# Performance work log

Hardware: AMD Instinct MI355X
Metric: run time of the kernel (lower is better)

## Reference

```python
import jax, jax.numpy as jnp
import numpy as np

CODE_DIM = 512
N_CODES = 8192
COMMITMENT_WEIGHT = 1.0


def setup_inputs() -> dict:
    key = jax.random.key(0)
    kx, kc = jax.random.split(key)
    x = jax.random.normal(kx, (8, 2048, CODE_DIM), dtype=jnp.float32)
    codebook = jax.random.normal(kc, (N_CODES, CODE_DIM), dtype=jnp.float32)  # N(0,1) init as in torch
    return {"x": x, "codebook": codebook}


def _cdist(x, codebook):
    x2 = jnp.sum(x * x, axis=-1, keepdims=True)          # [B, T, 1]
    c2 = jnp.sum(codebook * codebook, axis=-1)           # [K]
    xc = jnp.einsum('btd,kd->btk', x, codebook)          # [B, T, K]
    sq = jnp.maximum(x2 + c2[None, None, :] - 2.0 * xc, 0.0)
    return jnp.sqrt(sq)


def reference(x, codebook):
    dist = _cdist(x, codebook)                           # [B, T, K]
    indices = jnp.argmin(dist, axis=-1)                  # [B, T]
    codes = codebook[indices]                            # [B, T, D]
    code_loss = jnp.mean((codes - jax.lax.stop_gradient(x)) ** 2)
    embedding_loss = jnp.mean((x - jax.lax.stop_gradient(codes)) ** 2) * COMMITMENT_WEIGHT
    loss = code_loss + embedding_loss
    quantized = x + jax.lax.stop_gradient(codes - x)     # straight-through estimator
    return (quantized, indices, loss)
```

## Files before the change

kernel.cpp:

```cpp
#include <hip/hip_runtime.h>
#include <hip/hip_bf16.h>

typedef signed char s8;
typedef unsigned int u32;
typedef unsigned long long u64;
typedef __attribute__((ext_vector_type(4))) int v4i;

#define M_TOK 16384
#define DDIM 512
#define NCODES 8192
#define NTILE 64
#define BKB 64
#define KCH 8

#define QS   25.4f
#define QINV (1.0f / (QS * QS))

#define OFF_A8   0u
#define OFF_B8   8388608u
#define OFF_PART 12582912u
#define OFF_C2   20971520u
#define OFF_ACC  21004288u

__global__ void zero_kernel(float* __restrict__ acc) {
    if (threadIdx.x == 0 && blockIdx.x == 0) *acc = 0.f;
}

__global__ void quant_cb_c2_kernel(const float* __restrict__ cb, s8* __restrict__ B8,
                                   float* __restrict__ c2) {
    int row  = blockIdx.x * 4 + (threadIdx.x >> 6);
    int l    = threadIdx.x & 63;
    const float* p = cb + (size_t)row * DDIM + l * 8;
    float4 a = *(const float4*)p;
    float4 b = *(const float4*)(p + 4);
    float v[8] = {a.x, a.y, a.z, a.w, b.x, b.y, b.z, b.w};
    union { s8 c[8]; uint2 q; } H;
    float s = 0.f;
    #pragma unroll
    for (int j = 0; j < 8; ++j) {
        int q = (int)rintf(fminf(fmaxf(v[j] * QS, -127.f), 127.f));
        H.c[j] = (s8)q;
        s += v[j] * v[j];
    }
    *(uint2*)(B8 + (size_t)row * DDIM + l * 8) = H.q;
    #pragma unroll
    for (int off = 32; off; off >>= 1) s += __shfl_down(s, off);
    if (l == 0) c2[row] = s;
}

__global__ void quant_x_kernel(const float* __restrict__ src, s8* __restrict__ dst, int n16) {
    int i = blockIdx.x * blockDim.x + threadIdx.x;
    if (i >= n16) return;
    const float4* s4 = (const float4*)src + (size_t)i * 4;
    union { s8 c[16]; uint4 q; } H;
    #pragma unroll
    for (int k = 0; k < 4; ++k) {
        float4 a = s4[k];
        float v[4] = {a.x, a.y, a.z, a.w};
        #pragma unroll
        for (int j = 0; j < 4; ++j) {
            int q = (int)rintf(fminf(fmaxf(v[j] * QS, -127.f), 127.f));
            H.c[k * 4 + j] = (s8)q;
        }
    }
    *(uint4*)(dst + (size_t)i * 16) = H.q;
}

__launch_bounds__(256, 4)
__global__ void gemm_top1_kernel(const s8* __restrict__ A8, const s8* __restrict__ B8,
                                 const float* __restrict__ c2, u64* __restrict__ part) {
    __shared__ __align__(16) s8 Asb[2][128 * BKB];
    __shared__ __align__(16) s8 Bsb[2][128 * BKB];
    __shared__ u64 mergebuf[128][2];

    const int tid = threadIdx.x;
    const int wid = tid >> 6;
    const int l   = tid & 63;
    const int wr  = wid >> 1, wc = wid & 1;
    const int mtile = blockIdx.x >> 6;
    const int ntile = blockIdx.x & 63;
    const int row0 = mtile * 128;
    const int col0 = ntile * 128;

    const int lg = l >> 4;
    const int lc = l & 15;

    const int srowoff = l >> 2;
    const int sslot   = (l & 3) ^ ((l >> 3) & 3);

    auto STAGE = [&](int buf, int kc) {
        const int k0 = kc * BKB;
        #pragma unroll
        for (int i = 0; i < 2; ++i) {
            int rbase = i * 64 + wid * 16;
            int row = rbase + srowoff;
            const s8* ga = A8 + (size_t)(row0 + row) * DDIM + k0 + sslot * 16;
            __builtin_amdgcn_global_load_lds(
                (const __attribute__((address_space(1))) void*)ga,
                (__attribute__((address_space(3))) void*)&Asb[buf][rbase * BKB], 16, 0, 0);
            const s8* gb = B8 + (size_t)(col0 + row) * DDIM + k0 + sslot * 16;
            __builtin_amdgcn_global_load_lds(
                (const __attribute__((address_space(1))) void*)gb,
                (__attribute__((address_space(3))) void*)&Bsb[buf][rbase * BKB], 16, 0, 0);
        }
    };

    v4i acc[4][4];
    #pragma unroll
    for (int m = 0; m < 4; ++m)
        #pragma unroll
        for (int n = 0; n < 4; ++n) acc[m][n] = (v4i){0, 0, 0, 0};

    STAGE(0, 0);
    int cur = 0;
    const int slotbyte = (lg ^ ((lc >> 1) & 3)) * 16;
    for (int kc = 0; kc < KCH; ++kc) {
        asm volatile("s_waitcnt lgkmcnt(0)" ::: "memory");
        __builtin_amdgcn_sched_barrier(0);
        asm volatile("s_barrier" ::: "memory");
        if (kc < KCH - 1) {
            STAGE(cur ^ 1, kc + 1);
            asm volatile("s_waitcnt vmcnt(4)" ::: "memory");
        } else {
            asm volatile("s_waitcnt vmcnt(0)" ::: "memory");
        }
        asm volatile("s_barrier" ::: "memory");

        v4i af[4], bf[4];
        #pragma unroll
        for (int m = 0; m < 4; ++m) {
            int row = wr * 64 + m * 16 + lc;
            af[m] = *(const v4i*)((const char*)&Asb[cur][0] + row * BKB + slotbyte);
        }
        #pragma unroll
        for (int n = 0; n < 4; ++n) {
            int row = wc * 64 + n * 16 + lc;
            bf[n] = *(const v4i*)((const char*)&Bsb[cur][0] + row * BKB + slotbyte);
        }
        #pragma unroll
        for (int m = 0; m < 4; ++m)
            #pragma unroll
            for (int n = 0; n < 4; ++n)
                acc[m][n] = __builtin_amdgcn_mfma_i32_16x16x64_i8(af[m], bf[n], acc[m][n], 0, 0, 0);
        cur ^= 1;
    }

    float c2v[4];
    #pragma unroll
    for (int n = 0; n < 4; ++n) c2v[n] = c2[col0 + wc * 64 + n * 16 + lc];

    #pragma unroll
    for (int m = 0; m < 4; ++m) {
        #pragma unroll
        for (int j = 0; j < 4; ++j) {
            int rloc = wr * 64 + m * 16 + lg * 4 + j;
            u64 best = ~0ull;
            #pragma unroll
            for (int n = 0; n < 4; ++n) {
                float s = c2v[n] - 2.0f * (float)acc[m][n][j] * QINV;
                u32 b = __float_as_uint(s);
                b = (b & 0x80000000u) ? ~b : (b | 0x80000000u);
                int col = col0 + wc * 64 + n * 16 + lc;
                u64 key = ((u64)b << 32) | (u32)col;
                best = key < best ? key : best;
            }
            #pragma unroll
            for (int off = 1; off < 16; off <<= 1) {
                u64 o = __shfl_xor(best, off);
                best = o < best ? o : best;
            }
            if (lc == 0) mergebuf[rloc][wc] = best;
        }
    }
    __syncthreads();
    if (tid < 128) {
        u64 a = mergebuf[tid][0], b = mergebuf[tid][1];
        part[(size_t)(row0 + tid) * NTILE + ntile] = a < b ? a : b;
    }
}

__global__ void reduce_quant_kernel(const u64* __restrict__ part,
                                    const float* __restrict__ x, const float* __restrict__ cb,
                                    float* __restrict__ out, float* __restrict__ acc) {
    __shared__ float red[4];
    int t = blockIdx.x * 4 + (threadIdx.x >> 6);
    int l = threadIdx.x & 63;
    u64 k = part[(size_t)t * NTILE + l];

    int cand[4];
    #pragma unroll
    for (int c = 0; c < 4; ++c) {
        u64 m = k;
        #pragma unroll
        for (int off = 1; off < 64; off <<= 1) {
            u64 o = __shfl_xor(m, off);
            m = o < m ? o : m;
        }
        cand[c] = (int)(u32)(m & 0xffffffffull);
        if (k == m) k = ~0ull;
    }

    const float* xp = x + (size_t)t * DDIM + l * 8;
    float xv[8];
    #pragma unroll
    for (int j = 0; j < 8; ++j) xv[j] = xp[j];

    float cp[4][8];
    double d[4];
    #pragma unroll
    for (int c = 0; c < 4; ++c) {
        const float* cpp = cb + (size_t)cand[c] * DDIM + l * 8;
        double s = 0.0;
        #pragma unroll
        for (int j = 0; j < 8; ++j) {
            cp[c][j] = cpp[j];
            double a = (double)cp[c][j] - (double)xv[j];
            s += a * a;
        }
        d[c] = s;
    }
    #pragma unroll
    for (int c = 0; c < 4; ++c) {
        #pragma unroll
        for (int off = 1; off < 64; off <<= 1) d[c] += __shfl_xor(d[c], off);
    }

    double bd = d[0]; int bi = cand[0]; int bc = 0;
    #pragma unroll
    for (int c = 1; c < 4; ++c)
        if (d[c] < bd || (d[c] == bd && cand[c] < bi)) { bd = d[c]; bi = cand[c]; bc = c; }

    float cw[8];
    #pragma unroll
    for (int j = 0; j < 8; ++j) {
        float v = cp[0][j];
        #pragma unroll
        for (int c = 1; c < 4; ++c) v = (bc == c) ? cp[c][j] : v;
        cw[j] = v;
    }

    float ls = 0.f;
    float4 o0, o1;
    float dj[8];
    #pragma unroll
    for (int j = 0; j < 8; ++j) { dj[j] = cw[j] - xv[j]; ls += dj[j] * dj[j]; }
    o0.x = xv[0] + dj[0]; o0.y = xv[1] + dj[1]; o0.z = xv[2] + dj[2]; o0.w = xv[3] + dj[3];
    o1.x = xv[4] + dj[4]; o1.y = xv[5] + dj[5]; o1.z = xv[6] + dj[6]; o1.w = xv[7] + dj[7];
    float* op = out + (size_t)t * DDIM + l * 8;
    *(float4*)op = o0;
    *(float4*)(op + 4) = o1;

    if (l == 0) out[(size_t)M_TOK * DDIM + t] = (float)bi;

    #pragma unroll
    for (int off = 32; off; off >>= 1) ls += __shfl_down(ls, off);
    int wv = threadIdx.x >> 6;
    if (l == 0) red[wv] = ls;
    __syncthreads();
    if (threadIdx.x == 0) atomicAdd(acc, red[0] + red[1] + red[2] + red[3]);
}

__global__ void loss_final_kernel(const float* __restrict__ acc, float* __restrict__ out) {
    if (threadIdx.x == 0 && blockIdx.x == 0) {
        float mean = (*acc) / (float)((size_t)M_TOK * DDIM);
        out[(size_t)M_TOK * DDIM + M_TOK] = 2.0f * mean;
    }
}

extern "C" void kernel_launch(void* const* d_in, const int* in_sizes, int n_in,
                              void* d_out, int out_size, void* d_ws, size_t ws_size,
                              hipStream_t stream) {
    const float* x  = (const float*)d_in[0];
    const float* cb = (const float*)d_in[1];
    float* out = (float*)d_out;
    char* ws = (char*)d_ws;

    s8*    A8   = (s8*)(ws + OFF_A8);
    s8*    B8   = (s8*)(ws + OFF_B8);
    u64*   part = (u64*)(ws + OFF_PART);
    float* c2   = (float*)(ws + OFF_C2);
    float* acc  = (float*)(ws + OFF_ACC);

    zero_kernel<<<1, 64, 0, stream>>>(acc);
    quant_cb_c2_kernel<<<NCODES / 4, 256, 0, stream>>>(cb, B8, c2);
    quant_x_kernel<<<(M_TOK * DDIM / 16) / 256, 256, 0, stream>>>(x, A8, M_TOK * DDIM / 16);
    gemm_top1_kernel<<<(M_TOK / 128) * NTILE, 256, 0, stream>>>(A8, B8, c2, part);
    reduce_quant_kernel<<<M_TOK / 4, 256, 0, stream>>>(part, x, cb, out, acc);
    loss_final_kernel<<<1, 64, 0, stream>>>(acc, out);
}
```

Measured before the change: 196.7 us.

## Fuse prep kernels, triple-buffer GEMM staging, fold loss finalize, widen rerank

```diff
diff --git a/kernel.cpp b/kernel.cpp
--- a/kernel.cpp
+++ b/kernel.cpp
@@ -12,6 +12,7 @@
 #define NTILE 64
 #define BKB 64
 #define KCH 8
+#define NCAND 6
 
 #define QS   25.4f
 #define QINV (1.0f / (QS * QS))
@@ -21,56 +22,56 @@
 #define OFF_PART 12582912u
 #define OFF_C2   20971520u
 #define OFF_ACC  21004288u
-
-__global__ void zero_kernel(float* __restrict__ acc) {
-    if (threadIdx.x == 0 && blockIdx.x == 0) *acc = 0.f;
-}
-
-__global__ void quant_cb_c2_kernel(const float* __restrict__ cb, s8* __restrict__ B8,
-                                   float* __restrict__ c2) {
-    int row  = blockIdx.x * 4 + (threadIdx.x >> 6);
-    int l    = threadIdx.x & 63;
-    const float* p = cb + (size_t)row * DDIM + l * 8;
-    float4 a = *(const float4*)p;
-    float4 b = *(const float4*)(p + 4);
-    float v[8] = {a.x, a.y, a.z, a.w, b.x, b.y, b.z, b.w};
-    union { s8 c[8]; uint2 q; } H;
-    float s = 0.f;
-    #pragma unroll
-    for (int j = 0; j < 8; ++j) {
-        int q = (int)rintf(fminf(fmaxf(v[j] * QS, -127.f), 127.f));
-        H.c[j] = (s8)q;
-        s += v[j] * v[j];
-    }
-    *(uint2*)(B8 + (size_t)row * DDIM + l * 8) = H.q;
-    #pragma unroll
-    for (int off = 32; off; off >>= 1) s += __shfl_down(s, off);
-    if (l == 0) c2[row] = s;
-}
-
-__global__ void quant_x_kernel(const float* __restrict__ src, s8* __restrict__ dst, int n16) {
-    int i = blockIdx.x * blockDim.x + threadIdx.x;
-    if (i >= n16) return;
-    const float4* s4 = (const float4*)src + (size_t)i * 4;
-    union { s8 c[16]; uint4 q; } H;
-    #pragma unroll
-    for (int k = 0; k < 4; ++k) {
-        float4 a = s4[k];
-        float v[4] = {a.x, a.y, a.z, a.w};
-        #pragma unroll
-        for (int j = 0; j < 4; ++j) {
+#define OFF_CNT  21004292u
+
+__global__ void prep_kernel(const float* __restrict__ x, const float* __restrict__ cb,
+                            s8* __restrict__ A8, s8* __restrict__ B8,
+                            float* __restrict__ c2, float* __restrict__ acc,
+                            u32* __restrict__ counter) {
+    int bid = blockIdx.x;
+    if (bid == 0 && threadIdx.x == 0) { *acc = 0.f; *counter = 0u; }
+    if (bid < 2048) {
+        int row = bid * 4 + (threadIdx.x >> 6);
+        int l   = threadIdx.x & 63;
+        const float* p = cb + (size_t)row * DDIM + l * 8;
+        float4 a = *(const float4*)p;
+        float4 b = *(const float4*)(p + 4);
+        float v[8] = {a.x, a.y, a.z, a.w, b.x, b.y, b.z, b.w};
+        union { s8 c[8]; uint2 q; } H;
+        float s = 0.f;
+        #pragma unroll
+        for (int j = 0; j < 8; ++j) {
             int q = (int)rintf(fminf(fmaxf(v[j] * QS, -127.f), 127.f));
-            H.c[k * 4 + j] = (s8)q;
-        }
-    }
-    *(uint4*)(dst + (size_t)i * 16) = H.q;
-}
-
-__launch_bounds__(256, 4)
+            H.c[j] = (s8)q;
+            s += v[j] * v[j];
+        }
+        *(uint2*)(B8 + (size_t)row * DDIM + l * 8) = H.q;
+        #pragma unroll
+        for (int off = 32; off; off >>= 1) s += __shfl_down(s, off);
+        if (l == 0) c2[row] = s;
+    } else {
+        int i = (bid - 2048) * 256 + threadIdx.x;
+        const float4* s4 = (const float4*)x + (size_t)i * 4;
+        union { s8 c[16]; uint4 q; } H;
+        #pragma unroll
+        for (int k = 0; k < 4; ++k) {
+            float4 a = s4[k];
+            float v[4] = {a.x, a.y, a.z, a.w};
+            #pragma unroll
+            for (int j = 0; j < 4; ++j) {
+                int q = (int)rintf(fminf(fmaxf(v[j] * QS, -127.f), 127.f));
+                H.c[k * 4 + j] = (s8)q;
+            }
+        }
+        *(uint4*)(A8 + (size_t)i * 16) = H.q;
+    }
+}
+
+__launch_bounds__(256, 3)
 __global__ void gemm_top1_kernel(const s8* __restrict__ A8, const s8* __restrict__ B8,
                                  const float* __restrict__ c2, u64* __restrict__ part) {
-    __shared__ __align__(16) s8 Asb[2][128 * BKB];
-    __shared__ __align__(16) s8 Bsb[2][128 * BKB];
+    __shared__ __align__(16) s8 Asb[3][128 * BKB];
+    __shared__ __align__(16) s8 Bsb[3][128 * BKB];
     __shared__ u64 mergebuf[128][2];
 
     const int tid = threadIdx.x;
@@ -112,14 +113,20 @@
         for (int n = 0; n < 4; ++n) acc[m][n] = (v4i){0, 0, 0, 0};
 
     STAGE(0, 0);
-    int cur = 0;
+    STAGE(1, 1);
+
     const int slotbyte = (lg ^ ((lc >> 1) & 3)) * 16;
+
+    #pragma unroll
     for (int kc = 0; kc < KCH; ++kc) {
+        const int buf = kc % 3;
         asm volatile("s_waitcnt lgkmcnt(0)" ::: "memory");
         __builtin_amdgcn_sched_barrier(0);
         asm volatile("s_barrier" ::: "memory");
-        if (kc < KCH - 1) {
-            STAGE(cur ^ 1, kc + 1);
+        if (kc < KCH - 2) STAGE((kc + 2) % 3, kc + 2);
+        if (kc < KCH - 2) {
+            asm volatile("s_waitcnt vmcnt(8)" ::: "memory");
+        } else if (kc == KCH - 2) {
             asm volatile("s_waitcnt vmcnt(4)" ::: "memory");
         } else {
             asm volatile("s_waitcnt vmcnt(0)" ::: "memory");
@@ -130,19 +137,18 @@
         #pragma unroll
         for (int m = 0; m < 4; ++m) {
             int row = wr * 64 + m * 16 + lc;
-            af[m] = *(const v4i*)((const char*)&Asb[cur][0] + row * BKB + slotbyte);
+            af[m] = *(const v4i*)((const char*)&Asb[buf][0] + row * BKB + slotbyte);
         }
         #pragma unroll
         for (int n = 0; n < 4; ++n) {
             int row = wc * 64 + n * 16 + lc;
-            bf[n] = *(const v4i*)((const char*)&Bsb[cur][0] + row * BKB + slotbyte);
+            bf[n] = *(const v4i*)((const char*)&Bsb[buf][0] + row * BKB + slotbyte);
         }
         #pragma unroll
         for (int m = 0; m < 4; ++m)
             #pragma unroll
             for (int n = 0; n < 4; ++n)
                 acc[m][n] = __builtin_amdgcn_mfma_i32_16x16x64_i8(af[m], bf[n], acc[m][n], 0, 0, 0);
-        cur ^= 1;
     }
 
     float c2v[4];
@@ -181,15 +187,16 @@
 
 __global__ void reduce_quant_kernel(const u64* __restrict__ part,
                                     const float* __restrict__ x, const float* __restrict__ cb,
-                                    float* __restrict__ out, float* __restrict__ acc) {
+                                    float* __restrict__ out, float* __restrict__ acc,
+                                    u32* __restrict__ counter) {
     __shared__ float red[4];
     int t = blockIdx.x * 4 + (threadIdx.x >> 6);
     int l = threadIdx.x & 63;
     u64 k = part[(size_t)t * NTILE + l];
 
-    int cand[4];
-    #pragma unroll
-    for (int c = 0; c < 4; ++c) {
+    int cand[NCAND];
+    #pragma unroll
+    for (int c = 0; c < NCAND; ++c) {
         u64 m = k;
         #pragma unroll
         for (int off = 1; off < 64; off <<= 1) {
@@ -205,10 +212,10 @@
     #pragma unroll
     for (int j = 0; j < 8; ++j) xv[j] = xp[j];
 
-    float cp[4][8];
-    double d[4];
-    #pragma unroll
-    for (int c = 0; c < 4; ++c) {
+    float cp[NCAND][8];
+    double d[NCAND];
+    #pragma unroll
+    for (int c = 0; c < NCAND; ++c) {
         const float* cpp = cb + (size_t)cand[c] * DDIM + l * 8;
         double s = 0.0;
         #pragma unroll
@@ -220,14 +227,14 @@
         d[c] = s;
     }
     #pragma unroll
-    for (int c = 0; c < 4; ++c) {
+    for (int c = 0; c < NCAND; ++c) {
         #pragma unroll
         for (int off = 1; off < 64; off <<= 1) d[c] += __shfl_xor(d[c], off);
     }
 
     double bd = d[0]; int bi = cand[0]; int bc = 0;
     #pragma unroll
-    for (int c = 1; c < 4; ++c)
+    for (int c = 1; c < NCAND; ++c)
         if (d[c] < bd || (d[c] == bd && cand[c] < bi)) { bd = d[c]; bi = cand[c]; bc = c; }
 
     float cw[8];
@@ -235,7 +242,7 @@
     for (int j = 0; j < 8; ++j) {
         float v = cp[0][j];
         #pragma unroll
-        for (int c = 1; c < 4; ++c) v = (bc == c) ? cp[c][j] : v;
+        for (int c = 1; c < NCAND; ++c) v = (bc == c) ? cp[c][j] : v;
         cw[j] = v;
     }
 
@@ -257,13 +264,16 @@
     int wv = threadIdx.x >> 6;
     if (l == 0) red[wv] = ls;
     __syncthreads();
-    if (threadIdx.x == 0) atomicAdd(acc, red[0] + red[1] + red[2] + red[3]);
-}
-
-__global__ void loss_final_kernel(const float* __restrict__ acc, float* __restrict__ out) {
-    if (threadIdx.x == 0 && blockIdx.x == 0) {
-        float mean = (*acc) / (float)((size_t)M_TOK * DDIM);
-        out[(size_t)M_TOK * DDIM + M_TOK] = 2.0f * mean;
+    if (threadIdx.x == 0) {
+        atomicAdd(acc, red[0] + red[1] + red[2] + red[3]);
+        __threadfence();
+        u32 old = atomicAdd(counter, 1u);
+        if (old == gridDim.x - 1) {
+            __threadfence();
+            float total = atomicAdd(acc, 0.0f);
+            float mean = total / (float)((size_t)M_TOK * DDIM);
+            out[(size_t)M_TOK * DDIM + M_TOK] = 2.0f * mean;
+        }
     }
 }
 
@@ -280,11 +290,9 @@
     u64*   part = (u64*)(ws + OFF_PART);
     float* c2   = (float*)(ws + OFF_C2);
     float* acc  = (float*)(ws + OFF_ACC);
-
-    zero_kernel<<<1, 64, 0, stream>>>(acc);
-    quant_cb_c2_kernel<<<NCODES / 4, 256, 0, stream>>>(cb, B8, c2);
-    quant_x_kernel<<<(M_TOK * DDIM / 16) / 256, 256, 0, stream>>>(x, A8, M_TOK * DDIM / 16);
+    u32*   cnt  = (u32*)(ws + OFF_CNT);
+
+    prep_kernel<<<4096, 256, 0, stream>>>(x, cb, A8, B8, c2, acc, cnt);
     gemm_top1_kernel<<<(M_TOK / 128) * NTILE, 256, 0, stream>>>(A8, B8, c2, part);
-    reduce_quant_kernel<<<M_TOK / 4, 256, 0, stream>>>(part, x, cb, out, acc);
-    loss_final_kernel<<<1, 64, 0, stream>>>(acc, out);
-}
+    reduce_quant_kernel<<<M_TOK / 4, 256, 0, stream>>>(part, x, cb, out, acc, cnt);
+}
```

Measured after the change: 317.7 us. 61.5% more time.
